# Kernel tuning notes

Hardware: AMD Instinct MI355X
Metric: run time of the kernel (lower is better)

The kernel has to match this reference:

```python
import jax, jax.numpy as jnp
import numpy as np

Q = 128


def _maxpool2(x):
    # 2x2 max pool, stride 2, NCHW
    return jax.lax.reduce_window(x, -jnp.inf, jax.lax.max,
                                 (1, 1, 2, 2), (1, 1, 2, 2), 'VALID')


def _conv(x, w, b):
    y = jax.lax.conv_general_dilated(x, w, window_strides=(1, 1), padding='VALID',
                                     dimension_numbers=('NCHW', 'OIHW', 'NCHW'))
    return y + b[None, :, None, None]


def setup_inputs() -> dict:
    key = jax.random.key(0)
    ks = jax.random.split(key, 16)
    B = 4096
    x = jax.random.normal(ks[0], (B, 1, 28, 28), dtype=jnp.float32)
    hash_idx1 = jax.random.randint(ks[1], (25,), 0, Q, dtype=jnp.int32)
    hash_idx2 = jax.random.randint(ks[2], (800,), 0, Q, dtype=jnp.int32)
    hash_idx3 = jax.random.randint(ks[3], (1024,), 0, Q, dtype=jnp.int32)
    # random +/-1 signs
    sgn1 = jnp.sign(jax.random.normal(ks[4], (25,), dtype=jnp.float32))
    sgn2 = jnp.sign(jax.random.normal(ks[5], (800,), dtype=jnp.float32))
    sgn3 = jnp.sign(jax.random.normal(ks[6], (1024,), dtype=jnp.float32))
    # compressed (sketched) parameters: one length-Q vector per output unit
    w1 = jax.random.normal(ks[7], (32, Q), dtype=jnp.float32) * 0.2
    b1 = jax.random.normal(ks[8], (32,), dtype=jnp.float32) * 0.05
    w2 = jax.random.normal(ks[9], (64, Q), dtype=jnp.float32) * 0.05
    b2 = jax.random.normal(ks[10], (64,), dtype=jnp.float32) * 0.05
    w3 = jax.random.normal(ks[11], (512, Q), dtype=jnp.float32) * 0.03
    b3 = jax.random.normal(ks[12], (512,), dtype=jnp.float32) * 0.05
    fc2_w = jax.random.normal(ks[13], (10, 512), dtype=jnp.float32) * 0.04
    fc2_b = jax.random.normal(ks[14], (10,), dtype=jnp.float32) * 0.05
    return {'x': x,
            'hash_idx1': hash_idx1, 'hash_idx2': hash_idx2, 'hash_idx3': hash_idx3,
            'sgn1': sgn1, 'sgn2': sgn2, 'sgn3': sgn3,
            'w1': w1, 'b1': b1, 'w2': w2, 'b2': b2, 'w3': w3, 'b3': b3,
            'fc2_w': fc2_w, 'fc2_b': fc2_b}


def reference(x, hash_idx1, hash_idx2, hash_idx3, sgn1, sgn2, sgn3,
              w1, b1, w2, b2, w3, b3, fc2_w, fc2_b):
    # SketchConv1: reconstruct dense weight via gather + sign flip
    wc1 = (w1[:, hash_idx1] * sgn1[None, :]).reshape(32, 1, 5, 5)
    h = jax.nn.relu(_maxpool2(_conv(x, wc1, b1)))          # (B,32,12,12)
    # SketchConv2
    wc2 = (w2[:, hash_idx2] * sgn2[None, :]).reshape(64, 32, 5, 5)
    h = jax.nn.relu(_maxpool2(_conv(h, wc2, b2)))          # (B,64,4,4)
    h = h.reshape(h.shape[0], -1)                          # (B,1024)
    # SketchLinear
    W3 = w3[:, hash_idx3] * sgn3[None, :]                  # (512,1024)
    h = jax.nn.relu(h @ W3.T + b3)                         # (B,512)
    logits = h @ fc2_w.T + fc2_b                           # (B,10)
    return jax.nn.log_softmax(logits, axis=1)
```

## Files before the change

### kernel.cpp

```cpp
#include <hip/hip_runtime.h>
#include <hip/hip_bf16.h>
#include <math.h>


typedef __attribute__((ext_vector_type(8))) short bf16x8;
typedef __attribute__((ext_vector_type(4))) float f32x4;

static __device__ inline ushort f2bfu(float v) {
    union { __hip_bfloat16 h; ushort u; } cv;
    cv.h = __float2bfloat16(v);
    return cv.u;
}

static __device__ inline float bfu2f(ushort u) {
    union { ushort u; __hip_bfloat16 h; } cv;
    cv.u = u;
    return __bfloat162float(cv.h);
}


__global__ __launch_bounds__(256)
void k_reconstruct(const float* __restrict__ w1, const float* __restrict__ w2,
                   const float* __restrict__ w3,
                   const int* __restrict__ hi1, const int* __restrict__ hi2,
                   const int* __restrict__ hi3,
                   const float* __restrict__ s1, const float* __restrict__ s2,
                   __hip_bfloat16* __restrict__ wc1f,
                   __hip_bfloat16* __restrict__ wc1s,
                   __hip_bfloat16* __restrict__ wc2f,
                   __hip_bfloat16* __restrict__ W3d,
                   int* __restrict__ seg, int* __restrict__ pos) {
    if (blockIdx.x == 232) {
        __shared__ int scnt[128];
        __shared__ int sincl[128];
        __shared__ int sseg[129];
        const int u = threadIdx.x;
        if (u < 128) scnt[u] = 0;
        __syncthreads();
        int qq[4], rk[4];
        #pragma unroll
        for (int j = 0; j < 4; ++j) {
            int k = u * 4 + j;
            qq[j] = hi3[k];
            rk[j] = atomicAdd(&scnt[qq[j]], 1);
        }
        __syncthreads();
        if (u < 128) {
            int v = scnt[u];
            #pragma unroll
            for (int d = 1; d < 64; d <<= 1) {
                int t2 = __shfl_up(v, d);
                if ((u & 63) >= d) v += t2;
            }
            sincl[u] = v;
        }
        __syncthreads();
        if (u < 128) {
            int base = (u >= 64) ? sincl[63] : 0;
            sseg[u + 1] = base + sincl[u];
        }
        if (u == 0) sseg[0] = 0;
        __syncthreads();
        #pragma unroll
        for (int j = 0; j < 4; ++j) {
            int k = u * 4 + j;
            pos[k] = sseg[qq[j]] + rk[j];
        }
        if (u < 129) seg[u] = sseg[u];
        return;
    }
    const int t = blockIdx.x * blockDim.x + threadIdx.x;
    const int f = t >> 2;
    const int j0 = (t & 3) * 2;
    if (f < 256) {
        const bool shifted = f >= 128;
        const int u = f & 127;
        const int nt = u >> 6, lane = u & 63;
        const int quad = lane >> 4, l15 = lane & 15;
        const int oc = nt * 16 + l15;
        ushort rr[2];
        #pragma unroll
        for (int jj = 0; jj < 2; ++jj) {
            int tt = quad * 8 + j0 + jj;
            int ki = (tt * 43) >> 8;
            int kj = tt - 6 * ki;
            float v = 0.f;
            if (!shifted && ki < 5 && kj < 5) {
                int fi = ki * 5 + kj;
                v = w1[oc * 128 + hi1[fi]] * s1[fi];
            } else if (shifted && ki < 5 && kj >= 1 && kj <= 5) {
                int fi = ki * 5 + (kj - 1);
                v = w1[oc * 128 + hi1[fi]] * s1[fi];
            }
            rr[jj] = f2bfu(v);
        }
        *(uint*)((ushort*)(shifted ? wc1s : wc1f) + (size_t)u * 8 + j0) =
            (uint)rr[0] | ((uint)rr[1] << 16);
    } else if (f < 6656) {
        const int u = f - 256;
        const int l15 = u & 15, quad = (u >> 4) & 3;
        const int ntA = (u >> 6) & 3, tap = u >> 8;
        const int oc = ntA * 16 + l15;
        ushort rr[2];
        #pragma unroll
        for (int jj = 0; jj < 2; ++jj) {
            int ic = quad * 8 + j0 + jj;
            int fi = ic * 25 + tap;
            rr[jj] = f2bfu(w2[oc * 128 + hi2[fi]] * s2[fi]);
        }
        *(uint*)((ushort*)wc2f + (size_t)u * 8 + j0) =
            (uint)rr[0] | ((uint)rr[1] << 16);
    } else if (f < 14848) {
        const int u = f - 6656;
        const int l15 = u & 15, quad = (u >> 4) & 3;
        const int kt = (u >> 6) & 3, ntile = u >> 8;
        const int n = ntile * 16 + l15;
        ushort rr[2];
        #pragma unroll
        for (int jj = 0; jj < 2; ++jj) {
            int k = kt * 32 + quad * 8 + j0 + jj;
            rr[jj] = f2bfu(w3[n * 128 + k]);
        }
        *(uint*)((ushort*)W3d + (size_t)u * 8 + j0) =
            (uint)rr[0] | ((uint)rr[1] << 16);
    }
}

__global__ __launch_bounds__(512, 6)
void k_conv(const float* __restrict__ x,
            const __hip_bfloat16* __restrict__ wc1f,
            const __hip_bfloat16* __restrict__ wc1s,
            const __hip_bfloat16* __restrict__ wc2f,
            const float* __restrict__ b1, const float* __restrict__ b2,
            const int* __restrict__ pos, const float* __restrict__ s3,
            __hip_bfloat16* __restrict__ h2) {
    __shared__ __align__(16) ushort s_xb[4 * 816];
    __shared__ __align__(16) ushort s_h1[16 * 1160];

    const int tid = threadIdx.x;
    const int b0 = blockIdx.x * 4;
    const int wave = tid >> 6, lane = tid & 63;
    const int l15 = lane & 15, quad = lane >> 4;

    {
        const float4* xg = (const float4*)(x + (size_t)b0 * 784);
        for (int i = tid; i < 784; i += 512) {
            float4 v = xg[i];
            int img = i / 196;
            int p = (i - img * 196) * 4;
            ushort* dst = &s_xb[img * 816 + p];
            dst[0] = f2bfu(v.x); dst[1] = f2bfu(v.y);
            dst[2] = f2bfu(v.z); dst[3] = f2bfu(v.w);
        }
        if (tid < 128) {
            int img = tid >> 5, k = tid & 31;
            s_xb[img * 816 + 784 + k] = 0;
        }
    }

    bf16x8 bw1[2], bw1s[2];
    float bb1[2];
    #pragma unroll
    for (int nt = 0; nt < 2; ++nt) {
        bw1[nt]  = *(const bf16x8*)((const ushort*)wc1f + (nt * 64 + lane) * 8);
        bw1s[nt] = *(const bf16x8*)((const ushort*)wc1s + (nt * 64 + lane) * 8);
        bb1[nt] = b1[nt * 16 + l15];
    }
    __syncthreads();

    {
        const int img = wave >> 1, half = wave & 1;
        const int sub = l15 & 3;
        const ushort* srcImg = s_xb + img * 816;
        int offr[4];
        #pragma unroll
        for (int r = 0; r < 4; ++r) {
            int t = quad * 8 + 2 * r;
            int row = (t * 43) >> 8;
            int col = t - 6 * row;
            offr[r] = row * 28 + col;
        }
        const int g0 = l15 >> 3, r0 = l15 & 7;
        #pragma unroll
        for (int ii = 0; ii < 18; ++ii) {
            const int i = half * 18 + ii;
            const int pb = 4 * i + (l15 >> 2);
            const int pi = (pb * 171) >> 11;
            const int pj = pb - 12 * pi;
            const int base_e = (2 * pi + (sub >> 1)) * 28 + 2 * pj;
            const ushort* p0 = srcImg + base_e;
            union { bf16x8 v; uint u[4]; } A;
            A.u[0] = *(const uint*)(p0 + offr[0]);
            A.u[1] = *(const uint*)(p0 + offr[1]);
            A.u[2] = *(const uint*)(p0 + offr[2]);
            A.u[3] = *(const uint*)(p0 + offr[3]);
            f32x4 z = {0.f, 0.f, 0.f, 0.f};
            f32x4 ce0 = __builtin_amdgcn_mfma_f32_16x16x32_bf16(A.v, bw1[0],  z, 0, 0, 0);
            f32x4 co0 = __builtin_amdgcn_mfma_f32_16x16x32_bf16(A.v, bw1s[0], z, 0, 0, 0);
            f32x4 ce1 = __builtin_amdgcn_mfma_f32_16x16x32_bf16(A.v, bw1[1],  z, 0, 0, 0);
            f32x4 co1 = __builtin_amdgcn_mfma_f32_16x16x32_bf16(A.v, bw1s[1], z, 0, 0, 0);
            const int pbo = 4 * i + quad;
            float m0 = fmaxf(fmaxf(ce0[0], co0[1]), fmaxf(ce0[2], co0[3]));
            float m1 = fmaxf(fmaxf(ce1[0], co1[1]), fmaxf(ce1[2], co1[3]));
            s_h1[(img * 4 + g0) * 1160 + pbo * 8 + r0]     = f2bfu(fmaxf(m0 + bb1[0], 0.f));
            s_h1[(img * 4 + 2 + g0) * 1160 + pbo * 8 + r0] = f2bfu(fmaxf(m1 + bb1[1], 0.f));
        }
    }
    __syncthreads();

    const int pr = wave >> 1, nh = wave & 1;
    const int sub2 = l15 & 3;
    const int ci2 = 2 * pr + (sub2 >> 1);
    const int cj2 = 2 * (l15 >> 2) + (sub2 & 1);
    const int posBase = (ci2 * 12 + cj2) * 8;

    f32x4 acc[4][2];
    float bb2[2];
    #pragma unroll
    for (int ntl = 0; ntl < 2; ++ntl) {
        bb2[ntl] = b2[(nh * 2 + ntl) * 16 + l15];
        #pragma unroll
        for (int img = 0; img < 4; ++img)
            acc[img][ntl] = (f32x4){0.f, 0.f, 0.f, 0.f};
    }

    #pragma unroll
    for (int tap = 0; tap < 25; ++tap) {
        const int ki = tap / 5, kj = tap % 5;
        const int off = (ki * 12 + kj) * 8;
        bf16x8 a[4];
        #pragma unroll
        for (int img = 0; img < 4; ++img)
            a[img] = *(const bf16x8*)&s_h1[(img * 4 + quad) * 1160 + posBase + off];
        #pragma unroll
        for (int ntl = 0; ntl < 2; ++ntl) {
            bf16x8 bf = *(const bf16x8*)((const ushort*)wc2f +
                          ((tap * 4 + nh * 2 + ntl) * 64 + lane) * 8);
            #pragma unroll
            for (int img = 0; img < 4; ++img)
                acc[img][ntl] = __builtin_amdgcn_mfma_f32_16x16x32_bf16(
                    a[img], bf, acc[img][ntl], 0, 0, 0);
        }
    }

    const int k0 = ((nh * 2 + 0) * 16 + l15) * 16 + pr * 4 + quad;
    const int k1 = ((nh * 2 + 1) * 16 + l15) * 16 + pr * 4 + quad;
    const int p0 = pos[k0], p1 = pos[k1];
    const float sg0 = s3[k0], sg1 = s3[k1];
    #pragma unroll
    for (int img = 0; img < 4; ++img) {
        f32x4 c0 = acc[img][0];
        float m0 = fmaxf(fmaxf(c0[0], c0[1]), fmaxf(c0[2], c0[3]));
        float v0 = fmaxf(m0 + bb2[0], 0.f);
        h2[(size_t)(b0 + img) * 1024 + p0] = __float2bfloat16(v0 * sg0);
        f32x4 c1 = acc[img][1];
        float m1 = fmaxf(fmaxf(c1[0], c1[1]), fmaxf(c1[2], c1[3]));
        float v1 = fmaxf(m1 + bb2[1], 0.f);
        h2[(size_t)(b0 + img) * 1024 + p1] = __float2bfloat16(v1 * sg1);
    }
}

__global__ __launch_bounds__(1024)
void k_fc(const __hip_bfloat16* __restrict__ A, const __hip_bfloat16* __restrict__ W3d,
          const int* __restrict__ seg,
          const float* __restrict__ b3, const float* __restrict__ fc2w,
          const float* __restrict__ fc2b, float* __restrict__ out) {
    __shared__ __align__(16) ushort s_A[16 * 1032];
    __shared__ __align__(16) ushort s_Ab[16 * 136];
    __shared__ float s_h3[16 * 516];
    __shared__ int s_seg[132];

    const int tid = threadIdx.x;
    const int wave = tid >> 6, lane = tid & 63;
    const int l15 = lane & 15, quad = lane >> 4;
    const int mBase = blockIdx.x * 16;

    if (tid < 129) s_seg[tid] = seg[tid];
    {
        const uint4* g = (const uint4*)(A + (size_t)(mBase + wave) * 1024);
        uint4 v0 = g[lane * 2], v1 = g[lane * 2 + 1];
        uint4* d = (uint4*)&s_A[wave * 1032 + lane * 16];
        d[0] = v0; d[1] = v1;
    }
    __syncthreads();

    {
        const ushort* arow = &s_A[wave * 1032];
        const int q0 = lane * 2;
        const int a0 = s_seg[q0], e0 = s_seg[q0 + 1], e1 = s_seg[q0 + 2];
        const int n0 = e0 - a0, n1 = e1 - e0;
        const int nm = max(n0, n1);
        float v0 = 0.f, v1 = 0.f;
        for (int i = 0; i < nm; ++i) {
            if (i < n0) v0 += bfu2f(arow[a0 + i]);
            if (i < n1) v1 += bfu2f(arow[e0 + i]);
        }
        *(uint*)&s_Ab[wave * 136 + lane * 2] =
            (uint)f2bfu(v0) | ((uint)f2bfu(v1) << 16);
    }
    __syncthreads();

    f32x4 acc[2];
    acc[0] = (f32x4){0.f, 0.f, 0.f, 0.f};
    acc[1] = (f32x4){0.f, 0.f, 0.f, 0.f};

    const ushort* aP = &s_Ab[l15 * 136 + quad * 8];
    const ushort* bP0 = (const ushort*)W3d + ((size_t)(wave * 2)     * 4 * 64 + lane) * 8;
    const ushort* bP1 = (const ushort*)W3d + ((size_t)(wave * 2 + 1) * 4 * 64 + lane) * 8;
    #pragma unroll
    for (int kt = 0; kt < 4; ++kt) {
        bf16x8 a = *(const bf16x8*)(aP + kt * 32);
        bf16x8 bf0 = *(const bf16x8*)(bP0 + kt * 512);
        bf16x8 bf1 = *(const bf16x8*)(bP1 + kt * 512);
        acc[0] = __builtin_amdgcn_mfma_f32_16x16x32_bf16(a, bf0, acc[0], 0, 0, 0);
        acc[1] = __builtin_amdgcn_mfma_f32_16x16x32_bf16(a, bf1, acc[1], 0, 0, 0);
    }

    #pragma unroll
    for (int ntl = 0; ntl < 2; ++ntl) {
        int col = wave * 32 + ntl * 16 + l15;
        float bb = b3[col];
        #pragma unroll
        for (int r = 0; r < 4; ++r)
            s_h3[(quad * 4 + r) * 516 + col] = fmaxf(acc[ntl][r] + bb, 0.f);
    }
    __syncthreads();

    const float* hrow = &s_h3[wave * 516];
    float4 h0 = *(const float4*)&hrow[lane * 8];
    float4 h1 = *(const float4*)&hrow[lane * 8 + 4];
    float lg[10];
    #pragma unroll
    for (int c = 0; c < 10; ++c) {
        float4 w0 = *(const float4*)&fc2w[c * 512 + lane * 8];
        float4 w1 = *(const float4*)&fc2w[c * 512 + lane * 8 + 4];
        float s = h0.x * w0.x + h0.y * w0.y + h0.z * w0.z + h0.w * w0.w
                + h1.x * w1.x + h1.y * w1.y + h1.z * w1.z + h1.w * w1.w;
        s += __shfl_down(s, 32);
        s += __shfl_down(s, 16);
        s += __shfl_down(s, 8);
        s += __shfl_down(s, 4);
        s += __shfl_down(s, 2);
        s += __shfl_down(s, 1);
        lg[c] = s;
    }
    if (lane == 0) {
        float mx = -1e30f;
        #pragma unroll
        for (int c = 0; c < 10; ++c) { lg[c] += fc2b[c]; mx = fmaxf(mx, lg[c]); }
        float sum = 0.f;
        #pragma unroll
        for (int c = 0; c < 10; ++c) sum += expf(lg[c] - mx);
        float lse = mx + logf(sum);
        #pragma unroll
        for (int c = 0; c < 10; ++c)
            out[(size_t)(mBase + wave) * 10 + c] = lg[c] - lse;
    }
}

extern "C" void kernel_launch(void* const* d_in, const int* in_sizes, int n_in,
                              void* d_out, int out_size, void* d_ws, size_t ws_size,
                              hipStream_t stream) {
    const float* x    = (const float*)d_in[0];
    const int*   hi1  = (const int*)d_in[1];
    const int*   hi2  = (const int*)d_in[2];
    const int*   hi3  = (const int*)d_in[3];
    const float* s1   = (const float*)d_in[4];
    const float* s2   = (const float*)d_in[5];
    const float* s3   = (const float*)d_in[6];
    const float* w1   = (const float*)d_in[7];
    const float* b1   = (const float*)d_in[8];
    const float* w2   = (const float*)d_in[9];
    const float* b2   = (const float*)d_in[10];
    const float* w3   = (const float*)d_in[11];
    const float* b3   = (const float*)d_in[12];
    const float* fc2w = (const float*)d_in[13];
    const float* fc2b = (const float*)d_in[14];
    float* out = (float*)d_out;

    const int B = in_sizes[0] / 784;

    char* ws = (char*)d_ws;
    __hip_bfloat16* wc1f = (__hip_bfloat16*)(ws + 0);
    __hip_bfloat16* wc1s = (__hip_bfloat16*)(ws + 2048);
    __hip_bfloat16* wc2f = (__hip_bfloat16*)(ws + 4096);
    __hip_bfloat16* W3d  = (__hip_bfloat16*)(ws + 106496);
    int*            seg  = (int*)(ws + 237568);
    int*            pos  = (int*)(ws + 238592);
    __hip_bfloat16* h2   = (__hip_bfloat16*)(ws + 1155072);

    k_reconstruct<<<233, 256, 0, stream>>>(
        w1, w2, w3, hi1, hi2, hi3, s1, s2, wc1f, wc1s, wc2f, W3d, seg, pos);
    k_conv<<<B / 4, 512, 0, stream>>>(x, wc1f, wc1s, wc2f, b1, b2, pos, s3, h2);
    k_fc<<<B / 16, 1024, 0, stream>>>(h2, W3d, seg, b3, fc2w, fc2b, out);
}
```

Baseline: 135.7 us.

## Fuse hash-bucket segment reduction into conv epilogue, shrink intermediate to 128 per image

The conv kernel now scatters its pooled, signed outputs into shared memory and sums each hash-bucket segment there. It writes only 128 bf16 values per image instead of the 1024-wide permuted activation. The FC kernel loads the compact 128-wide rows directly and no longer does the segment reduction. This removes most of the global write and read traffic for the intermediate h2, at the cost of two extra block barriers and a serial per-thread segment loop in the conv kernel.

New measurement: 128.8 us (median of 2 runs). -5.1%, faster.

```diff
diff --git a/kernel.cpp b/kernel.cpp
--- a/kernel.cpp
+++ b/kernel.cpp
@@ -132,7 +132,8 @@
             const __hip_bfloat16* __restrict__ wc1s,
             const __hip_bfloat16* __restrict__ wc2f,
             const float* __restrict__ b1, const float* __restrict__ b2,
-            const int* __restrict__ pos, const float* __restrict__ s3,
+            const int* __restrict__ pos, const int* __restrict__ seg,
+            const float* __restrict__ s3,
             __hip_bfloat16* __restrict__ h2) {
     __shared__ __align__(16) ushort s_xb[4 * 816];
     __shared__ __align__(16) ushort s_h1[16 * 1160];
@@ -243,60 +244,53 @@
         }
     }
 
-    const int k0 = ((nh * 2 + 0) * 16 + l15) * 16 + pr * 4 + quad;
-    const int k1 = ((nh * 2 + 1) * 16 + l15) * 16 + pr * 4 + quad;
-    const int p0 = pos[k0], p1 = pos[k1];
-    const float sg0 = s3[k0], sg1 = s3[k1];
-    #pragma unroll
-    for (int img = 0; img < 4; ++img) {
-        f32x4 c0 = acc[img][0];
-        float m0 = fmaxf(fmaxf(c0[0], c0[1]), fmaxf(c0[2], c0[3]));
-        float v0 = fmaxf(m0 + bb2[0], 0.f);
-        h2[(size_t)(b0 + img) * 1024 + p0] = __float2bfloat16(v0 * sg0);
-        f32x4 c1 = acc[img][1];
-        float m1 = fmaxf(fmaxf(c1[0], c1[1]), fmaxf(c1[2], c1[3]));
-        float v1 = fmaxf(m1 + bb2[1], 0.f);
-        h2[(size_t)(b0 + img) * 1024 + p1] = __float2bfloat16(v1 * sg1);
+    __syncthreads();
+
+    ushort* s_hs = s_h1;
+    {
+        const int k0 = ((nh * 2 + 0) * 16 + l15) * 16 + pr * 4 + quad;
+        const int k1 = ((nh * 2 + 1) * 16 + l15) * 16 + pr * 4 + quad;
+        const int p0 = pos[k0], p1 = pos[k1];
+        const float sg0 = s3[k0], sg1 = s3[k1];
+        #pragma unroll
+        for (int img = 0; img < 4; ++img) {
+            f32x4 c0 = acc[img][0];
+            float m0 = fmaxf(fmaxf(c0[0], c0[1]), fmaxf(c0[2], c0[3]));
+            float v0 = fmaxf(m0 + bb2[0], 0.f);
+            s_hs[img * 1024 + p0] = f2bfu(v0 * sg0);
+            f32x4 c1 = acc[img][1];
+            float m1 = fmaxf(fmaxf(c1[0], c1[1]), fmaxf(c1[2], c1[3]));
+            float v1 = fmaxf(m1 + bb2[1], 0.f);
+            s_hs[img * 1024 + p1] = f2bfu(v1 * sg1);
+        }
+    }
+    __syncthreads();
+
+    {
+        const int img = tid >> 7, q = tid & 127;
+        const int a0 = seg[q], n = seg[q + 1] - a0;
+        const ushort* src = s_hs + img * 1024 + a0;
+        float v = 0.f;
+        for (int i = 0; i < n; ++i) v += bfu2f(src[i]);
+        h2[(size_t)(b0 + img) * 128 + q] = __float2bfloat16(v);
     }
 }
 
 __global__ __launch_bounds__(1024)
 void k_fc(const __hip_bfloat16* __restrict__ A, const __hip_bfloat16* __restrict__ W3d,
-          const int* __restrict__ seg,
           const float* __restrict__ b3, const float* __restrict__ fc2w,
           const float* __restrict__ fc2b, float* __restrict__ out) {
-    __shared__ __align__(16) ushort s_A[16 * 1032];
-    __shared__ __align__(16) ushort s_Ab[16 * 136];
+    __shared__ __align__(16) ushort s_A[16 * 136];
     __shared__ float s_h3[16 * 516];
-    __shared__ int s_seg[132];
 
     const int tid = threadIdx.x;
     const int wave = tid >> 6, lane = tid & 63;
     const int l15 = lane & 15, quad = lane >> 4;
     const int mBase = blockIdx.x * 16;
 
-    if (tid < 129) s_seg[tid] = seg[tid];
-    {
-        const uint4* g = (const uint4*)(A + (size_t)(mBase + wave) * 1024);
-        uint4 v0 = g[lane * 2], v1 = g[lane * 2 + 1];
-        uint4* d = (uint4*)&s_A[wave * 1032 + lane * 16];
-        d[0] = v0; d[1] = v1;
-    }
-    __syncthreads();
-
-    {
-        const ushort* arow = &s_A[wave * 1032];
-        const int q0 = lane * 2;
-        const int a0 = s_seg[q0], e0 = s_seg[q0 + 1], e1 = s_seg[q0 + 2];
-        const int n0 = e0 - a0, n1 = e1 - e0;
-        const int nm = max(n0, n1);
-        float v0 = 0.f, v1 = 0.f;
-        for (int i = 0; i < nm; ++i) {
-            if (i < n0) v0 += bfu2f(arow[a0 + i]);
-            if (i < n1) v1 += bfu2f(arow[e0 + i]);
-        }
-        *(uint*)&s_Ab[wave * 136 + lane * 2] =
-            (uint)f2bfu(v0) | ((uint)f2bfu(v1) << 16);
+    {
+        const uint* g = (const uint*)(A + (size_t)(mBase + wave) * 128);
+        *(uint*)&s_A[wave * 136 + lane * 2] = g[lane];
     }
     __syncthreads();
 
@@ -304,7 +298,7 @@
     acc[0] = (f32x4){0.f, 0.f, 0.f, 0.f};
     acc[1] = (f32x4){0.f, 0.f, 0.f, 0.f};
 
-    const ushort* aP = &s_Ab[l15 * 136 + quad * 8];
+    const ushort* aP = &s_A[l15 * 136 + quad * 8];
     const ushort* bP0 = (const ushort*)W3d + ((size_t)(wave * 2)     * 4 * 64 + lane) * 8;
     const ushort* bP1 = (const ushort*)W3d + ((size_t)(wave * 2 + 1) * 4 * 64 + lane) * 8;
     #pragma unroll
@@ -391,6 +385,6 @@
 
     k_reconstruct<<<233, 256, 0, stream>>>(
         w1, w2, w3, hi1, hi2, hi3, s1, s2, wc1f, wc1s, wc2f, W3d, seg, pos);
-    k_conv<<<B / 4, 512, 0, stream>>>(x, wc1f, wc1s, wc2f, b1, b2, pos, s3, h2);
-    k_fc<<<B / 16, 1024, 0, stream>>>(h2, W3d, seg, b3, fc2w, fc2b, out);
-}
+    k_conv<<<B / 4, 512, 0, stream>>>(x, wc1f, wc1s, wc2f, b1, b2, pos, seg, s3, h2);
+    k_fc<<<B / 16, 1024, 0, stream>>>(h2, W3d, b3, fc2w, fc2b, out);
+}
```
